# Optimization experiments

Measured on AMD Instinct MI355X. Metric: run time of the kernel, lower is better.

The kernel has to match this reference:

```python
import jax, jax.numpy as jnp
import numpy as np

N = 4096
IN_F = 256
OUT_F = 64
HEADS = 4
EDGE_F = 32
ALPHA = 0.2  # leaky relu negative slope


def setup_inputs() -> dict:
    key = jax.random.key(0)
    k1, k2, k3, k4, k5 = jax.random.split(key, 5)
    h = jax.random.normal(k1, (N, IN_F), dtype=jnp.float32)
    adj = jax.random.randint(k2, (N, N, 1), 0, 2, dtype=jnp.int32)
    edge_attr = jax.random.normal(k3, (N, EDGE_F), dtype=jnp.float32)
    # xavier-uniform-ish params
    W = jax.random.normal(k4, (IN_F, HEADS * OUT_F), dtype=jnp.float32) * 0.1
    a = jax.random.normal(k5, (HEADS, 2 * OUT_F + EDGE_F, 1), dtype=jnp.float32) * 0.1
    return {"h": h, "adj": adj, "edge_attr": edge_attr, "W": W, "a": a}


def reference(h, adj, edge_attr, W, a):
    n = h.shape[0]
    Wh = (h @ W).reshape(n, HEADS, OUT_F)            # [N, H, O]
    a_vec = a[:, :, 0]                               # [H, 2O+E]
    a_src = a_vec[:, :OUT_F]                         # [H, O]
    a_dst = a_vec[:, OUT_F:2 * OUT_F]                # [H, O]
    a_edge = a_vec[:, 2 * OUT_F:]                    # [H, E]
    # decompose the all-pairs concat dot-product: score(i,j,h) =
    #   a_src.Wh[i] + a_dst.Wh[j] + a_edge.edge_attr[j]  (edge term follows repeat(N,1) semantics)
    src = jnp.einsum('nho,ho->nh', Wh, a_src)        # [N, H]
    dst = jnp.einsum('nho,ho->nh', Wh, a_dst)        # [N, H]
    edg = jnp.einsum('ne,he->nh', edge_attr, a_edge) # [N, H]
    e = jax.nn.leaky_relu(src[:, None, :] + (dst + edg)[None, :, :],
                          negative_slope=ALPHA)       # [N, N, H]
    att = jnp.where(adj > 0, e, jnp.zeros((), e.dtype))
    att = jax.nn.softmax(att, axis=1)                # softmax over neighbors j
    # dropout p=0.0 (eval): no-op
    h_prime = jnp.einsum('ijh,jho->iho', att, Wh)    # [N, H, O]
    return jax.nn.elu(h_prime.reshape(n, HEADS * OUT_F))
```

## Files before the change

### kernel.cpp

```cpp
#include <hip/hip_runtime.h>
#include <hip/hip_bf16.h>
#include <math.h>

#define NN 4096
#define IN_F 256
#define OUT_F 64
#define HEADS 4
#define EDGE_F 32
#define HO 256
#define AVEC 160
#define ALPHA 0.2f
#define LOG2E 1.44269504088896f

typedef __attribute__((ext_vector_type(8))) short bf16x8;
typedef __attribute__((ext_vector_type(4))) float f32x4;

__device__ __forceinline__ float exp2fast(float x) {
    return __builtin_amdgcn_exp2f(x);
}

__device__ __forceinline__ unsigned short f2bf(float x) {
    unsigned u = __float_as_uint(x);
    u += 0x7FFF + ((u >> 16) & 1);
    return (unsigned short)(u >> 16);
}

__global__ __launch_bounds__(256) void k_pack(const int* __restrict__ adj,
                                              unsigned* __restrict__ abitsT) {
    __shared__ unsigned bits[32][16];
    const int tid = threadIdx.x;
    const int w = tid >> 6, l = tid & 63;
    const int ib = blockIdx.x >> 2, js = blockIdx.x & 3;
    const int i0 = ib * 16;
    const int jbase = js * 1024 + w * 256;
    const int* base = adj + (size_t)i0 * NN + jbase + l;

#pragma unroll
    for (int half = 0; half < 2; ++half) {
        int vv[32];
#pragma unroll
        for (int t = 0; t < 32; ++t) {
            const int ii = (t & 7) + half * 8;
            const int r = t >> 3;
            vv[t] = base[(size_t)ii * NN + r * 64];
        }
#pragma unroll
        for (int t = 0; t < 32; ++t) {
            const int ii = (t & 7) + half * 8;
            const int r = t >> 3;
            const unsigned long long m = __ballot(vv[t] > 0);
            const int jwl = w * 8 + r * 2;
            if (l == 0) bits[jwl][ii] = (unsigned)m;
            else if (l == 1) bits[jwl + 1][ii] = (unsigned)(m >> 32);
        }
    }
    __syncthreads();
#pragma unroll
    for (int t = tid; t < 32 * 16; t += 256) {
        const int jwl = t >> 4, ii = t & 15;
        abitsT[(size_t)(js * 32 + jwl) * NN + i0 + ii] = bits[jwl][ii];
    }
}

__global__ __launch_bounds__(256) void k_wh(const float* __restrict__ h,
                                            const float* __restrict__ W,
                                            const float* __restrict__ a,
                                            const float* __restrict__ edge_attr,
                                            unsigned short* __restrict__ pk,
                                            float* __restrict__ src,
                                            float* __restrict__ cdpT) {
    __shared__ float hs[32][32];
    __shared__ float Ws[32][64];
    const int tid = threadIdx.x;
    const int jb = blockIdx.x >> 2, hd = blockIdx.x & 3;
    const int n0 = jb * 32;
    const int rg = tid >> 6, cl = tid & 63;
    float acc[8];
#pragma unroll
    for (int r = 0; r < 8; ++r) acc[r] = 0.f;

    for (int kc = 0; kc < IN_F; kc += 32) {
        {
            const int r = tid >> 3, k4 = (tid & 7) << 2;
            *(float4*)&hs[r][k4] = *(const float4*)&h[(size_t)(n0 + r) * IN_F + kc + k4];
        }
#pragma unroll
        for (int q = 0; q < 2; ++q) {
            const int f = tid + q * 256;
            const int k = f >> 4, c4 = (f & 15) << 2;
            *(float4*)&Ws[k][c4] = *(const float4*)&W[(size_t)(kc + k) * HO + hd * 64 + c4];
        }
        __syncthreads();
#pragma unroll
        for (int k = 0; k < 32; ++k) {
            const float wv = Ws[k][cl];
#pragma unroll
            for (int r = 0; r < 8; ++r)
                acc[r] = fmaf(hs[rg * 8 + r][k], wv, acc[r]);
        }
        __syncthreads();
    }

    {
        const int g = cl >> 4, lr = cl & 15;
        unsigned short* fb = pk + ((size_t)(jb * HEADS + hd) * 4 + g) * 512;
        bf16x8 v;
#pragma unroll
        for (int r = 0; r < 8; ++r) v[r] = (short)f2bf(acc[r]);
        *(bf16x8*)(fb + (rg * 16 + lr) * 8) = v;
    }

    const float asrc = a[hd * AVEC + cl];
    const float adst = a[hd * AVEC + OUT_F + cl];
    float s_keep = 0.f, d_keep = 0.f;
#pragma unroll
    for (int r = 0; r < 8; ++r) {
        float sp = acc[r] * asrc;
        float dp = acc[r] * adst;
#pragma unroll
        for (int off = 32; off >= 1; off >>= 1) {
            sp += __shfl_xor(sp, off);
            dp += __shfl_xor(dp, off);
        }
        if (cl == r) { s_keep = sp; d_keep = dp; }
    }
    if (cl < 8) {
        const int i = n0 + rg * 8 + cl;
        float eg = 0.f;
        const float* erow = edge_attr + (size_t)i * EDGE_F;
#pragma unroll
        for (int e4 = 0; e4 < EDGE_F; e4 += 4) {
            const float4 ev = *(const float4*)(erow + e4);
            const float4 av = *(const float4*)(a + hd * AVEC + 2 * OUT_F + e4);
            eg = fmaf(ev.x, av.x, fmaf(ev.y, av.y, fmaf(ev.z, av.z, fmaf(ev.w, av.w, eg))));
        }
        src[i * HEADS + hd] = s_keep * LOG2E;
        cdpT[(size_t)hd * NN + i] = (d_keep + eg) * LOG2E;
    }
}

__global__ __launch_bounds__(512, 4) void k_pv(const unsigned* __restrict__ abitsT,
                                               const unsigned short* __restrict__ pk,
                                               const float* __restrict__ src,
                                               const float* __restrict__ cdpT,
                                               float* __restrict__ out) {
    __shared__ float plds[4][32][65];
    __shared__ float lsum[4][32];
    const int tid = threadIdx.x;
    const int w = tid >> 6, l = tid & 63;
    const int js = w & 3, mt = w >> 2;
    const int ib = blockIdx.x >> 2, hd = blockIdx.x & 3;
    const int i0 = ib * 32;
    const int lr = l & 15, kb = l >> 4;
    const int i = i0 + mt * 16 + lr;
    const float si = src[i * HEADS + hd];
    const float* crow = cdpT + (size_t)hd * NN + kb * 8;
    const unsigned short* pkb = pk + (size_t)hd * 2048 + l * 8;

    bf16x8 bones;
#pragma unroll
    for (int r = 0; r < 8; ++r) bones[r] = (short)0x3F80;

    f32x4 acc0 = {0.f, 0.f, 0.f, 0.f};
    f32x4 acc1 = {0.f, 0.f, 0.f, 0.f};
    f32x4 acc2 = {0.f, 0.f, 0.f, 0.f};
    f32x4 acc3 = {0.f, 0.f, 0.f, 0.f};
    f32x4 accL = {0.f, 0.f, 0.f, 0.f};

    for (int jt = js * 32; jt < NN; jt += 128) {
        const unsigned wbits = abitsT[(size_t)(jt >> 5) * NN + i];
        const unsigned byte = (wbits >> (kb * 8)) & 0xFFu;
        const float4 c0 = *(const float4*)(crow + jt);
        const float4 c1 = *(const float4*)(crow + jt + 4);
        const unsigned short* fb = pkb + (size_t)(jt >> 5) * (HEADS * 4 * 512);
        const bf16x8 b0 = *(const bf16x8*)(fb);
        const bf16x8 b1 = *(const bf16x8*)(fb + 512);
        const bf16x8 b2 = *(const bf16x8*)(fb + 1024);
        const bf16x8 b3 = *(const bf16x8*)(fb + 1536);
        float e, p0, p1, p2, p3, p4, p5, p6, p7;
        e = si + c0.x; e = fmaxf(e, ALPHA * e); e = (byte &   1u) ? e : 0.f; p0 = exp2fast(e);
        e = si + c0.y; e = fmaxf(e, ALPHA * e); e = (byte &   2u) ? e : 0.f; p1 = exp2fast(e);
        e = si + c0.z; e = fmaxf(e, ALPHA * e); e = (byte &   4u) ? e : 0.f; p2 = exp2fast(e);
        e = si + c0.w; e = fmaxf(e, ALPHA * e); e = (byte &   8u) ? e : 0.f; p3 = exp2fast(e);
        e = si + c1.x; e = fmaxf(e, ALPHA * e); e = (byte &  16u) ? e : 0.f; p4 = exp2fast(e);
        e = si + c1.y; e = fmaxf(e, ALPHA * e); e = (byte &  32u) ? e : 0.f; p5 = exp2fast(e);
        e = si + c1.z; e = fmaxf(e, ALPHA * e); e = (byte &  64u) ? e : 0.f; p6 = exp2fast(e);
        e = si + c1.w; e = fmaxf(e, ALPHA * e); e = (byte & 128u) ? e : 0.f; p7 = exp2fast(e);
        bf16x8 af;
        af[0] = (short)f2bf(p0); af[1] = (short)f2bf(p1);
        af[2] = (short)f2bf(p2); af[3] = (short)f2bf(p3);
        af[4] = (short)f2bf(p4); af[5] = (short)f2bf(p5);
        af[6] = (short)f2bf(p6); af[7] = (short)f2bf(p7);
        acc0 = __builtin_amdgcn_mfma_f32_16x16x32_bf16(af, b0, acc0, 0, 0, 0);
        acc1 = __builtin_amdgcn_mfma_f32_16x16x32_bf16(af, b1, acc1, 0, 0, 0);
        acc2 = __builtin_amdgcn_mfma_f32_16x16x32_bf16(af, b2, acc2, 0, 0, 0);
        acc3 = __builtin_amdgcn_mfma_f32_16x16x32_bf16(af, b3, acc3, 0, 0, 0);
        accL = __builtin_amdgcn_mfma_f32_16x16x32_bf16(af, bones, accL, 0, 0, 0);
    }

    if (lr == 0) {
#pragma unroll
        for (int r = 0; r < 4; ++r)
            lsum[js][mt * 16 + kb * 4 + r] = accL[r];
    }
#pragma unroll
    for (int r = 0; r < 4; ++r) {
        const int row = mt * 16 + kb * 4 + r;
        plds[js][row][ 0 + lr] = acc0[r];
        plds[js][row][16 + lr] = acc1[r];
        plds[js][row][32 + lr] = acc2[r];
        plds[js][row][48 + lr] = acc3[r];
    }
    __syncthreads();

    const int row = tid >> 4, c4 = (tid & 15) << 2;
    const float L = lsum[0][row] + lsum[1][row] + lsum[2][row] + lsum[3][row];
    const float inv = 1.f / L;
    float4 o;
    float x;
    x = (plds[0][row][c4 + 0] + plds[1][row][c4 + 0] + plds[2][row][c4 + 0] + plds[3][row][c4 + 0]) * inv;
    o.x = x > 0.f ? x : (__expf(x) - 1.f);
    x = (plds[0][row][c4 + 1] + plds[1][row][c4 + 1] + plds[2][row][c4 + 1] + plds[3][row][c4 + 1]) * inv;
    o.y = x > 0.f ? x : (__expf(x) - 1.f);
    x = (plds[0][row][c4 + 2] + plds[1][row][c4 + 2] + plds[2][row][c4 + 2] + plds[3][row][c4 + 2]) * inv;
    o.z = x > 0.f ? x : (__expf(x) - 1.f);
    x = (plds[0][row][c4 + 3] + plds[1][row][c4 + 3] + plds[2][row][c4 + 3] + plds[3][row][c4 + 3]) * inv;
    o.w = x > 0.f ? x : (__expf(x) - 1.f);
    *(float4*)(out + (size_t)(i0 + row) * HO + hd * 64 + c4) = o;
}

extern "C" void kernel_launch(void* const* d_in, const int* in_sizes, int n_in,
                              void* d_out, int out_size, void* d_ws, size_t ws_size,
                              hipStream_t stream) {
    const float* h         = (const float*)d_in[0];
    const int*   adj       = (const int*)d_in[1];
    const float* edge_attr = (const float*)d_in[2];
    const float* W         = (const float*)d_in[3];
    const float* a         = (const float*)d_in[4];
    float* out = (float*)d_out;

    unsigned short* pk     = (unsigned short*)d_ws;
    float*          cdpT   = (float*)(pk + (size_t)NN * HO);
    float*          src    = cdpT + (size_t)HEADS * NN;
    unsigned*       abitsT = (unsigned*)(src + (size_t)NN * HEADS);

    k_pack<<<256 * 4, 256, 0, stream>>>(adj, abitsT);
    k_wh<<<128 * HEADS, 256, 0, stream>>>(h, W, a, edge_attr, pk, src, cdpT);
    k_pv<<<128 * HEADS, 512, 0, stream>>>(abitsT, pk, src, cdpT, out);
}
```

Measured before the change: 173.4 us.

## Split PV kernel into 16-row tiles with 8-way neighbor split-K

Reworks the attention-PV kernel so each block handles 16 query rows per head instead of 32. All 8 waves now split the neighbor dimension rather than 4 splits by 2 row tiles, which doubles the grid to 1024 blocks and raises the occupancy hint. The aim is more blocks to fill the CUs and hide memory latency. In exchange, each key/value fragment from pk and cdpT is loaded twice as many times across blocks, and the LDS reduction over 8 partials costs more.

```diff
diff --git a/kernel.cpp b/kernel.cpp
--- a/kernel.cpp
+++ b/kernel.cpp
@@ -139,20 +139,19 @@
     }
 }
 
-__global__ __launch_bounds__(512, 4) void k_pv(const unsigned* __restrict__ abitsT,
+__global__ __launch_bounds__(512, 8) void k_pv(const unsigned* __restrict__ abitsT,
                                                const unsigned short* __restrict__ pk,
                                                const float* __restrict__ src,
                                                const float* __restrict__ cdpT,
                                                float* __restrict__ out) {
-    __shared__ float plds[4][32][65];
-    __shared__ float lsum[4][32];
+    __shared__ float plds[8][16][65];
+    __shared__ float lsum[8][16];
     const int tid = threadIdx.x;
-    const int w = tid >> 6, l = tid & 63;
-    const int js = w & 3, mt = w >> 2;
+    const int js = tid >> 6, l = tid & 63;
     const int ib = blockIdx.x >> 2, hd = blockIdx.x & 3;
-    const int i0 = ib * 32;
+    const int i0 = ib * 16;
     const int lr = l & 15, kb = l >> 4;
-    const int i = i0 + mt * 16 + lr;
+    const int i = i0 + lr;
     const float si = src[i * HEADS + hd];
     const float* crow = cdpT + (size_t)hd * NN + kb * 8;
     const unsigned short* pkb = pk + (size_t)hd * 2048 + l * 8;
@@ -167,7 +166,7 @@
     f32x4 acc3 = {0.f, 0.f, 0.f, 0.f};
     f32x4 accL = {0.f, 0.f, 0.f, 0.f};
 
-    for (int jt = js * 32; jt < NN; jt += 128) {
+    for (int jt = js * 32; jt < NN; jt += 256) {
         const unsigned wbits = abitsT[(size_t)(jt >> 5) * NN + i];
         const unsigned byte = (wbits >> (kb * 8)) & 0xFFu;
         const float4 c0 = *(const float4*)(crow + jt);
@@ -201,11 +200,11 @@
     if (lr == 0) {
 #pragma unroll
         for (int r = 0; r < 4; ++r)
-            lsum[js][mt * 16 + kb * 4 + r] = accL[r];
+            lsum[js][kb * 4 + r] = accL[r];
     }
 #pragma unroll
     for (int r = 0; r < 4; ++r) {
-        const int row = mt * 16 + kb * 4 + r;
+        const int row = kb * 4 + r;
         plds[js][row][ 0 + lr] = acc0[r];
         plds[js][row][16 + lr] = acc1[r];
         plds[js][row][32 + lr] = acc2[r];
@@ -213,20 +212,20 @@
     }
     __syncthreads();
 
-    const int row = tid >> 4, c4 = (tid & 15) << 2;
-    const float L = lsum[0][row] + lsum[1][row] + lsum[2][row] + lsum[3][row];
+    const int row = tid >> 5, cp = (tid & 31) * 2;
+    float L = 0.f, x0 = 0.f, x1 = 0.f;
+#pragma unroll
+    for (int p = 0; p < 8; ++p) {
+        L  += lsum[p][row];
+        x0 += plds[p][row][cp];
+        x1 += plds[p][row][cp + 1];
+    }
     const float inv = 1.f / L;
-    float4 o;
+    float2 o;
     float x;
-    x = (plds[0][row][c4 + 0] + plds[1][row][c4 + 0] + plds[2][row][c4 + 0] + plds[3][row][c4 + 0]) * inv;
-    o.x = x > 0.f ? x : (__expf(x) - 1.f);
-    x = (plds[0][row][c4 + 1] + plds[1][row][c4 + 1] + plds[2][row][c4 + 1] + plds[3][row][c4 + 1]) * inv;
-    o.y = x > 0.f ? x : (__expf(x) - 1.f);
-    x = (plds[0][row][c4 + 2] + plds[1][row][c4 + 2] + plds[2][row][c4 + 2] + plds[3][row][c4 + 2]) * inv;
-    o.z = x > 0.f ? x : (__expf(x) - 1.f);
-    x = (plds[0][row][c4 + 3] + plds[1][row][c4 + 3] + plds[2][row][c4 + 3] + plds[3][row][c4 + 3]) * inv;
-    o.w = x > 0.f ? x : (__expf(x) - 1.f);
-    *(float4*)(out + (size_t)(i0 + row) * HO + hd * 64 + c4) = o;
+    x = x0 * inv; o.x = x > 0.f ? x : (__expf(x) - 1.f);
+    x = x1 * inv; o.y = x > 0.f ? x : (__expf(x) - 1.f);
+    *(float2*)(out + (size_t)(i0 + row) * HO + hd * 64 + cp) = o;
 }
 
 extern "C" void kernel_launch(void* const* d_in, const int* in_sizes, int n_in,
@@ -246,5 +245,5 @@
 
     k_pack<<<256 * 4, 256, 0, stream>>>(adj, abitsT);
     k_wh<<<128 * HEADS, 256, 0, stream>>>(h, W, a, edge_attr, pk, src, cdpT);
-    k_pv<<<128 * HEADS, 512, 0, stream>>>(abitsT, pk, src, cdpT, out);
-}
+    k_pv<<<256 * 4, 512, 0, stream>>>(abitsT, pk, src, cdpT, out);
+}
```

Result: faster. 157.6 us (-9.1%).
